# Optimization experiments

Measured on AMD Instinct MI355X. Metric: run time of the kernel, lower is better.

## Reference

```python
import jax, jax.numpy as jnp
import numpy as np

TEMPERATURE = 1.0
N_NODES = 50000
N_EDGES = 1600000
BATCH = 2
C_IN = 64
C_OUT = 64


def setup_inputs() -> dict:
    key = jax.random.key(0)
    k = jax.random.split(key, 8)
    # edge_index with no self-loops: tgt = (src + 1 + off) % N, off in [0, N-2)
    src = jax.random.randint(k[0], (N_EDGES,), 0, N_NODES, dtype=jnp.int64)
    off = jax.random.randint(k[1], (N_EDGES,), 0, N_NODES - 1, dtype=jnp.int64)
    tgt = (src + 1 + off) % N_NODES
    edge_index = jnp.stack([src, tgt])  # (2, E)
    x = jax.random.normal(k[2], (BATCH, N_NODES, C_IN), dtype=jnp.float32)
    f_disc_orig = jax.random.uniform(k[3], (N_EDGES,), dtype=jnp.float32)
    fluxes = jax.random.normal(k[4], (BATCH, N_NODES), dtype=jnp.float32)
    W_conc = jax.random.normal(k[5], (C_OUT, C_IN), dtype=jnp.float32) * (1.0 / np.sqrt(C_IN))
    W_disc = jax.random.normal(k[6], (C_OUT, C_IN), dtype=jnp.float32) * (1.0 / np.sqrt(C_IN))
    bias = jnp.zeros((C_OUT,), dtype=jnp.float32)
    return {"x": x, "edge_index": edge_index, "f_disc_orig": f_disc_orig,
            "fluxes": fluxes, "W_conc": W_conc, "W_disc": W_disc, "bias": bias}


def reference(x, edge_index, f_disc_orig, fluxes, W_conc, W_disc, bias):
    B, N, _ = x.shape
    src0, tgt0 = edge_index[0], edge_index[1]  # original edges (no self-loops)
    loops = jnp.arange(N, dtype=edge_index.dtype)
    src = jnp.concatenate([src0, loops])  # (E+N,)
    tgt = jnp.concatenate([tgt0, loops])
    # GCN symmetric normalization D^{-1/2} A D^{-1/2} (with self-loops)
    deg = jnp.zeros((N,), x.dtype).at[tgt].add(1.0)
    dis = jnp.where(deg > 0, jax.lax.rsqrt(jnp.maximum(deg, 1e-30)), 0.0)
    norm = dis[src] * dis[tgt]  # (E+N,)
    # dynamic discordant strength on original (non-self-loop) edges
    sign_prod = jnp.tanh(fluxes[:, src0] * fluxes[:, tgt0] / TEMPERATURE)  # (B, E)
    keep = (1.0 + sign_prod) * 0.5
    fdo = f_disc_orig[None, :]
    f_disc = keep * fdo + (1.0 - keep) * (1.0 - fdo)  # (B, E)
    # self-loop messages are purely concordant (f_disc = 0)
    f_full = jnp.concatenate([f_disc, jnp.zeros((B, N), x.dtype)], axis=1)  # (B, E+N)
    # transform once per node, then gather per edge
    xc = jnp.einsum('bni,oi->bno', x, W_conc)  # (B, N, O)
    xd = jnp.einsum('bni,oi->bno', x, W_disc)
    msg = norm[None, :, None] * ((1.0 - f_full)[..., None] * xc[:, src] +
                                 f_full[..., None] * xd[:, src])  # (B, E+N, O)
    out = jnp.zeros((B, N, xc.shape[-1]), x.dtype).at[:, tgt].add(msg)
    return out + bias
```

## Files before the change

kernel.cpp:

```cpp
#include <hip/hip_runtime.h>
#include <math.h>


constexpr int C = 64;
constexpr int CNB = 128;
constexpr int CCAP = 5120;

typedef short short8 __attribute__((ext_vector_type(8)));
typedef float f32x4 __attribute__((ext_vector_type(4)));

__device__ __forceinline__ unsigned pack_bf16x2(float a, float b) {
    unsigned ua = __float_as_uint(a);
    ua = (ua + 0x7fffu + ((ua >> 16) & 1u)) >> 16;
    unsigned ub = __float_as_uint(b);
    ub = (ub + 0x7fffu + ((ub >> 16) & 1u)) >> 16;
    return ua | (ub << 16);
}
__device__ __forceinline__ float bflo(unsigned p) { return __uint_as_float(p << 16); }
__device__ __forceinline__ float bfhi(unsigned p) { return __uint_as_float(p & 0xffff0000u); }

__global__ __launch_bounds__(256) void convert_kernel(
    const float* __restrict__ x, unsigned* __restrict__ xb2, int nwords,
    int* __restrict__ coarseCursor, int ncoarse) {
    int i = blockIdx.x * blockDim.x + threadIdx.x;
    if (i < ncoarse) coarseCursor[i] = 0;
    int stride = gridDim.x * blockDim.x;
    const float2* x2 = (const float2*)x;
    for (int w = i; w < nwords; w += stride) {
        float2 xv = x2[w];
        xb2[w] = pack_bf16x2(xv.x, xv.y);
    }
}

__global__ __launch_bounds__(256) void binA1_kernel(
    const int* __restrict__ src, const int* __restrict__ tgt,
    const float* __restrict__ fdo, int* __restrict__ coarseCursor,
    unsigned long long* __restrict__ slab, int E, int ncoarse) {
    __shared__ int hcnt[512];
    __shared__ int hbase[512];
    const int tid = threadIdx.x;
    const int chunk0 = blockIdx.x * 8192;
    for (int c = tid; c < 512; c += 256) hcnt[c] = 0;
    __syncthreads();
#pragma unroll 4
    for (int k = 0; k < 32; ++k) {
        int e = chunk0 + tid + k * 256;
        if (e < E) atomicAdd(&hcnt[tgt[e] >> 7], 1);
    }
    __syncthreads();
    for (int c = tid; c < ncoarse; c += 256) {
        int cc = hcnt[c];
        hbase[c] = cc ? atomicAdd(&coarseCursor[c], cc) : 0;
        hcnt[c] = 0;
    }
    __syncthreads();
#pragma unroll 4
    for (int k = 0; k < 32; ++k) {
        int e = chunk0 + tid + k * 256;
        if (e < E) {
            int t = tgt[e];
            int b = t >> 7;
            int pos = hbase[b] + atomicAdd(&hcnt[b], 1);
            if (pos < CCAP) {
                unsigned q = (unsigned)(fdo[e] * 32767.0f + 0.5f);
                unsigned long long en = (unsigned long long)(unsigned)src[e]
                                      | ((unsigned long long)(unsigned)(t & 127) << 17)
                                      | ((unsigned long long)q << 24);
                slab[(size_t)b * CCAP + pos] = en;
            }
        }
    }
}

__global__ __launch_bounds__(1024) void binA2_kernel(
    const unsigned long long* __restrict__ slab,
    const int* __restrict__ coarseCursor, const float* __restrict__ flux,
    unsigned* __restrict__ epackFine, float4* __restrict__ nodeinfo, int N) {
    const int b = blockIdx.x;
    const int tid = threadIdx.x;
    __shared__ int ncnt[CNB];
    __shared__ int nsc[CNB];
    __shared__ int ncur[CNB];
    int cnt = min(coarseCursor[b], CCAP);
    if (tid < CNB) { ncnt[tid] = 0; ncur[tid] = 0; }
    __syncthreads();
    const unsigned long long* sl = slab + (size_t)b * CCAP;
    for (int i = tid; i < cnt; i += 1024)
        atomicAdd(&ncnt[(int)((sl[i] >> 17) & 127)], 1);
    __syncthreads();
    if (tid < CNB) nsc[tid] = ncnt[tid];
    __syncthreads();
    for (int off = 1; off < CNB; off <<= 1) {
        int v = (tid < CNB && tid >= off) ? nsc[tid - off] : 0;
        __syncthreads();
        if (tid < CNB) nsc[tid] += v;
        __syncthreads();
    }
    for (int i = tid; i < cnt; i += 1024) {
        unsigned long long e = sl[i];
        int s = (int)(e & 0x1FFFFull);
        int tl = (int)((e >> 17) & 127);
        unsigned q = (unsigned)((e >> 24) & 0x7FFF);
        int pos = nsc[tl] - ncnt[tl] + atomicAdd(&ncur[tl], 1);
        epackFine[(size_t)b * CCAP + pos] = (unsigned)s | (q << 17);
    }
    if (tid < CNB) {
        int n = b * CNB + tid;
        if (n < N) {
            int dg = ncnt[tid];
            int rs = b * CCAP + (nsc[tid] - dg);
            float4 ni;
            ni.x = rsqrtf((float)(dg + 1));
            ni.y = flux[n];
            ni.z = flux[N + n];
            ni.w = __int_as_float((dg << 21) | rs);
            nodeinfo[n] = ni;
        }
    }
}

__global__ __launch_bounds__(256) void aggregate_kernel(
    const float4* __restrict__ nodeinfo, const unsigned* __restrict__ epackFine,
    const unsigned* __restrict__ xb2, unsigned* __restrict__ up,
    unsigned* __restrict__ vp, int N) {
    const int lane = threadIdx.x & 63;
    const int wslot = threadIdx.x >> 6;
    const int node = blockIdx.x * 4 + wslot;
    __shared__ float4 s_e[4][2][64];
    if (node >= N) return;
    const int e2 = lane >> 4;
    const int q16 = lane & 15;
    const int g = q16 >> 3;
    const int p = q16 & 7;
    float4 ni = nodeinfo[node];
    const unsigned wbits = (unsigned)__float_as_int(ni.w);
    const int start = (int)(wbits & 0x1FFFFFu);
    const int end = start + (int)(wbits >> 21);
    const float dt = ni.x, f0t = ni.y, f1t = ni.z;
    const char* xbg = (const char*)xb2 + (size_t)g * N * 128 + p * 16;
    float au[8] = {0, 0, 0, 0, 0, 0, 0, 0};
    float av[8] = {0, 0, 0, 0, 0, 0, 0, 0};
    for (int base = start; base < end; base += 64) {
        int cnt = min(64, end - base);
        int cntp = (cnt + 3) & ~3;
        if (lane < cnt) {
            unsigned pe = epackFine[base + lane];
            int s = (int)(pe & 0x1FFFFu);
            float fd = (float)(pe >> 17) * (1.0f / 32767.0f);
            float4 nis = nodeinfo[s];
            float nrm = nis.x * dt;
            float p0 = nis.y * f0t;
            float p1 = nis.z * f1t;
            float k0 = 1.0f / (1.0f + __expf(-2.0f * p0));
            float k1 = 1.0f / (1.0f + __expf(-2.0f * p1));
            float w = 2.0f * fd - 1.0f;
            float f0 = fmaf(k0, w, 1.0f - fd);
            float f1 = fmaf(k1, w, 1.0f - fd);
            float soff = __int_as_float(s << 7);
            s_e[wslot][0][lane] = make_float4(soff, nrm * (1.0f - f0), nrm * f0, 0.f);
            s_e[wslot][1][lane] = make_float4(soff, nrm * (1.0f - f1), nrm * f1, 0.f);
        } else if (lane < cntp) {
            float4 z = make_float4(0.f, 0.f, 0.f, 0.f);
            s_e[wslot][0][lane] = z;
            s_e[wslot][1][lane] = z;
        }
        float4 r0 = s_e[wslot][g][e2];
        uint4 xwN = *(const uint4*)(xbg + __float_as_int(r0.x));
        float ccN = r0.y, cdN = r0.z;
        for (int j = 4; j < cntp; j += 4) {
            uint4 xw = xwN;
            float cc = ccN, cd = cdN;
            float4 r2 = s_e[wslot][g][j + e2];
            xwN = *(const uint4*)(xbg + __float_as_int(r2.x));
            ccN = r2.y; cdN = r2.z;
#pragma unroll
            for (int w = 0; w < 4; ++w) {
                unsigned xp = (&xw.x)[w];
                float lo = bflo(xp), hi = bfhi(xp);
                au[2 * w] = fmaf(cc, lo, au[2 * w]);
                au[2 * w + 1] = fmaf(cc, hi, au[2 * w + 1]);
                av[2 * w] = fmaf(cd, lo, av[2 * w]);
                av[2 * w + 1] = fmaf(cd, hi, av[2 * w + 1]);
            }
        }
#pragma unroll
        for (int w = 0; w < 4; ++w) {
            unsigned xp = (&xwN.x)[w];
            float lo = bflo(xp), hi = bfhi(xp);
            au[2 * w] = fmaf(ccN, lo, au[2 * w]);
            au[2 * w + 1] = fmaf(ccN, hi, au[2 * w + 1]);
            av[2 * w] = fmaf(cdN, lo, av[2 * w]);
            av[2 * w + 1] = fmaf(cdN, hi, av[2 * w + 1]);
        }
    }
#pragma unroll
    for (int k = 0; k < 8; ++k) {
        au[k] += __shfl_xor(au[k], 16, 64);
        au[k] += __shfl_xor(au[k], 32, 64);
        av[k] += __shfl_xor(av[k], 16, 64);
        av[k] += __shfl_xor(av[k], 32, 64);
    }
    if (e2 == 0) {
        uint4 xs = *(const uint4*)(xbg + ((size_t)node << 7));
        float d2 = dt * dt;
#pragma unroll
        for (int w = 0; w < 4; ++w) {
            unsigned xp = (&xs.x)[w];
            au[2 * w] = fmaf(d2, bflo(xp), au[2 * w]);
            au[2 * w + 1] = fmaf(d2, bfhi(xp), au[2 * w + 1]);
        }
        uint4 uo, vo;
        uo.x = pack_bf16x2(au[0], au[1]);
        uo.y = pack_bf16x2(au[2], au[3]);
        uo.z = pack_bf16x2(au[4], au[5]);
        uo.w = pack_bf16x2(au[6], au[7]);
        vo.x = pack_bf16x2(av[0], av[1]);
        vo.y = pack_bf16x2(av[2], av[3]);
        vo.z = pack_bf16x2(av[4], av[5]);
        vo.w = pack_bf16x2(av[6], av[7]);
        size_t wo = ((size_t)(g * N + node)) * 32 + 4 * p;
        *(uint4*)(up + wo) = uo;
        *(uint4*)(vp + wo) = vo;
    }
}

__device__ __forceinline__ short8 make_bfrag(const float* __restrict__ row, int off) {
    const float4* p = (const float4*)(row + off);
    float4 lo = p[0], hi = p[1];
    uint4 w;
    w.x = pack_bf16x2(lo.x, lo.y);
    w.y = pack_bf16x2(lo.z, lo.w);
    w.z = pack_bf16x2(hi.x, hi.y);
    w.w = pack_bf16x2(hi.z, hi.w);
    return __builtin_bit_cast(short8, w);
}

__global__ __launch_bounds__(256) void gemm_mfma_kernel(
    const unsigned* __restrict__ up, const unsigned* __restrict__ vp,
    const float* __restrict__ Wc, const float* __restrict__ Wd,
    const float* __restrict__ bias, float* __restrict__ out, int ntiles) {
    const int lane = threadIdx.x & 63;
    const int nl = lane & 15;
    const int quad = lane >> 4;
    const int wave = blockIdx.x * 4 + (threadIdx.x >> 6);
    const int nwaves = gridDim.x * 4;

    short8 bf[4][4];
    float bt[4];
#pragma unroll
    for (int t = 0; t < 4; ++t) {
        int n = 16 * t + nl;
        const float* wcr = Wc + n * 64;
        const float* wdr = Wd + n * 64;
        bf[0][t] = make_bfrag(wcr, quad * 8);
        bf[1][t] = make_bfrag(wcr, 32 + quad * 8);
        bf[2][t] = make_bfrag(wdr, quad * 8);
        bf[3][t] = make_bfrag(wdr, 32 + quad * 8);
        bt[t] = bias[n];
    }

    for (int tile = wave; tile < ntiles; tile += nwaves) {
        int row = tile * 16 + nl;
        const uint4* ur = (const uint4*)(up + (size_t)row * 32);
        const uint4* vr = (const uint4*)(vp + (size_t)row * 32);
        short8 a0 = __builtin_bit_cast(short8, ur[quad]);
        short8 a1 = __builtin_bit_cast(short8, ur[4 + quad]);
        short8 a2 = __builtin_bit_cast(short8, vr[quad]);
        short8 a3 = __builtin_bit_cast(short8, vr[4 + quad]);
        f32x4 acc[4];
#pragma unroll
        for (int t = 0; t < 4; ++t) {
            f32x4 z = {0.f, 0.f, 0.f, 0.f};
            acc[t] = __builtin_amdgcn_mfma_f32_16x16x32_bf16(a0, bf[0][t], z, 0, 0, 0);
            acc[t] = __builtin_amdgcn_mfma_f32_16x16x32_bf16(a1, bf[1][t], acc[t], 0, 0, 0);
            acc[t] = __builtin_amdgcn_mfma_f32_16x16x32_bf16(a2, bf[2][t], acc[t], 0, 0, 0);
            acc[t] = __builtin_amdgcn_mfma_f32_16x16x32_bf16(a3, bf[3][t], acc[t], 0, 0, 0);
        }
        float* ob = out + ((size_t)(tile * 16 + quad * 4) << 6);
#pragma unroll
        for (int t = 0; t < 4; ++t) {
            int col = 16 * t + nl;
#pragma unroll
            for (int r = 0; r < 4; ++r)
                ob[(r << 6) + col] = acc[t][r] + bt[t];
        }
    }
}

extern "C" void kernel_launch(void* const* d_in, const int* in_sizes, int n_in,
                              void* d_out, int out_size, void* d_ws, size_t ws_size,
                              hipStream_t stream) {
    const float* x = (const float*)d_in[0];
    const int* ei = (const int*)d_in[1];
    const float* fdo = (const float*)d_in[2];
    const float* flux = (const float*)d_in[3];
    const float* Wc = (const float*)d_in[4];
    const float* Wd = (const float*)d_in[5];
    const float* bias = (const float*)d_in[6];
    float* out = (float*)d_out;

    const int E = in_sizes[2];
    const int BN = in_sizes[3];
    const int N = BN / 2;
    const int ncoarse = (N + CNB - 1) / CNB;

    auto align = [](size_t o) { return (o + 255) & ~(size_t)255; };
    char* ws = (char*)d_ws;
    size_t o = 0;
    int* coarseCursor = (int*)(ws + o);            o = align(o + (size_t)ncoarse * 4);
    float4* nodeinfo = (float4*)(ws + o);          o = align(o + (size_t)N * 16);
    unsigned long long* slab = (unsigned long long*)(ws + o);
    unsigned* up = (unsigned*)slab;
    o = align(o + (size_t)ncoarse * CCAP * 8);
    unsigned* epackFine = (unsigned*)(ws + o);     o = align(o + (size_t)ncoarse * CCAP * 4);
    unsigned* xb2 = (unsigned*)(ws + o);           o = align(o + (size_t)BN * 32 * 4);
    unsigned* vp = (unsigned*)(ws + o);            o += (size_t)BN * 32 * 4;

    const int* srcp = ei;
    const int* tgtp = ei + E;

    convert_kernel<<<2048, 256, 0, stream>>>(x, xb2, BN * 32, coarseCursor, ncoarse);
    binA1_kernel<<<(E + 8191) / 8192, 256, 0, stream>>>(srcp, tgtp, fdo,
                                                        coarseCursor, slab, E, ncoarse);
    binA2_kernel<<<ncoarse, 1024, 0, stream>>>(slab, coarseCursor, flux,
                                               epackFine, nodeinfo, N);
    aggregate_kernel<<<(N + 3) / 4, 256, 0, stream>>>(nodeinfo, epackFine, xb2,
                                                      up, vp, N);
    gemm_mfma_kernel<<<512, 256, 0, stream>>>(up, vp, Wc, Wd, bias, out, BN / 16);
}
```

Measured before the change: 220.7 us.

## Interleave batch bf16 rows per node, double gather ILP, shrink blocks

The convert kernel now writes both batch copies of each node contiguously (256 bytes per node), so the two batch gathers in the aggregate kernel hit one contiguous region instead of two distant rows. The aggregate loop processes two edge groups per iteration with two outstanding gather loads, and padding becomes a multiple of 8, to raise memory-level parallelism. Block sizes drop to 128 threads for aggregation and 256 for the fine binning kernel. The convert kernel's reads become strided across batches, and the binning loops run more iterations per thread.

Measured after the change: 225.3 us. 2.1% more time.

```diff
diff --git a/kernel.cpp b/kernel.cpp
--- a/kernel.cpp
+++ b/kernel.cpp
@@ -20,14 +20,18 @@
 __device__ __forceinline__ float bfhi(unsigned p) { return __uint_as_float(p & 0xffff0000u); }
 
 __global__ __launch_bounds__(256) void convert_kernel(
-    const float* __restrict__ x, unsigned* __restrict__ xb2, int nwords,
+    const float* __restrict__ x, unsigned* __restrict__ xb2, int N,
     int* __restrict__ coarseCursor, int ncoarse) {
     int i = blockIdx.x * blockDim.x + threadIdx.x;
     if (i < ncoarse) coarseCursor[i] = 0;
     int stride = gridDim.x * blockDim.x;
     const float2* x2 = (const float2*)x;
+    int nwords = N * 64;
     for (int w = i; w < nwords; w += stride) {
-        float2 xv = x2[w];
+        int node = w >> 6;
+        int g = (w >> 5) & 1;
+        int c = w & 31;
+        float2 xv = x2[((size_t)(g * N + node)) * 32 + c];
         xb2[w] = pack_bf16x2(xv.x, xv.y);
     }
 }
@@ -72,7 +76,7 @@
     }
 }
 
-__global__ __launch_bounds__(1024) void binA2_kernel(
+__global__ __launch_bounds__(256) void binA2_kernel(
     const unsigned long long* __restrict__ slab,
     const int* __restrict__ coarseCursor, const float* __restrict__ flux,
     unsigned* __restrict__ epackFine, float4* __restrict__ nodeinfo, int N) {
@@ -85,7 +89,7 @@
     if (tid < CNB) { ncnt[tid] = 0; ncur[tid] = 0; }
     __syncthreads();
     const unsigned long long* sl = slab + (size_t)b * CCAP;
-    for (int i = tid; i < cnt; i += 1024)
+    for (int i = tid; i < cnt; i += 256)
         atomicAdd(&ncnt[(int)((sl[i] >> 17) & 127)], 1);
     __syncthreads();
     if (tid < CNB) nsc[tid] = ncnt[tid];
@@ -96,7 +100,7 @@
         if (tid < CNB) nsc[tid] += v;
         __syncthreads();
     }
-    for (int i = tid; i < cnt; i += 1024) {
+    for (int i = tid; i < cnt; i += 256) {
         unsigned long long e = sl[i];
         int s = (int)(e & 0x1FFFFull);
         int tl = (int)((e >> 17) & 127);
@@ -119,14 +123,14 @@
     }
 }
 
-__global__ __launch_bounds__(256) void aggregate_kernel(
+__global__ __launch_bounds__(128) void aggregate_kernel(
     const float4* __restrict__ nodeinfo, const unsigned* __restrict__ epackFine,
     const unsigned* __restrict__ xb2, unsigned* __restrict__ up,
     unsigned* __restrict__ vp, int N) {
     const int lane = threadIdx.x & 63;
     const int wslot = threadIdx.x >> 6;
-    const int node = blockIdx.x * 4 + wslot;
-    __shared__ float4 s_e[4][2][64];
+    const int node = blockIdx.x * 2 + wslot;
+    __shared__ float4 s_e[2][2][64];
     if (node >= N) return;
     const int e2 = lane >> 4;
     const int q16 = lane & 15;
@@ -137,12 +141,13 @@
     const int start = (int)(wbits & 0x1FFFFFu);
     const int end = start + (int)(wbits >> 21);
     const float dt = ni.x, f0t = ni.y, f1t = ni.z;
-    const char* xbg = (const char*)xb2 + (size_t)g * N * 128 + p * 16;
+    const char* xbase = (const char*)xb2;
+    const int lane_off = g * 128 + p * 16;
     float au[8] = {0, 0, 0, 0, 0, 0, 0, 0};
     float av[8] = {0, 0, 0, 0, 0, 0, 0, 0};
     for (int base = start; base < end; base += 64) {
         int cnt = min(64, end - base);
-        int cntp = (cnt + 3) & ~3;
+        int cntp = (cnt + 7) & ~7;
         if (lane < cnt) {
             unsigned pe = epackFine[base + lane];
             int s = (int)(pe & 0x1FFFFu);
@@ -156,7 +161,7 @@
             float w = 2.0f * fd - 1.0f;
             float f0 = fmaf(k0, w, 1.0f - fd);
             float f1 = fmaf(k1, w, 1.0f - fd);
-            float soff = __int_as_float(s << 7);
+            float soff = __int_as_float(s << 8);
             s_e[wslot][0][lane] = make_float4(soff, nrm * (1.0f - f0), nrm * f0, 0.f);
             s_e[wslot][1][lane] = make_float4(soff, nrm * (1.0f - f1), nrm * f1, 0.f);
         } else if (lane < cntp) {
@@ -164,33 +169,54 @@
             s_e[wslot][0][lane] = z;
             s_e[wslot][1][lane] = z;
         }
-        float4 r0 = s_e[wslot][g][e2];
-        uint4 xwN = *(const uint4*)(xbg + __float_as_int(r0.x));
-        float ccN = r0.y, cdN = r0.z;
-        for (int j = 4; j < cntp; j += 4) {
-            uint4 xw = xwN;
-            float cc = ccN, cd = cdN;
-            float4 r2 = s_e[wslot][g][j + e2];
-            xwN = *(const uint4*)(xbg + __float_as_int(r2.x));
-            ccN = r2.y; cdN = r2.z;
+        float4 rA = s_e[wslot][g][e2];
+        float4 rB = s_e[wslot][g][4 + e2];
+        uint4 xwA = *(const uint4*)(xbase + (size_t)(unsigned)__float_as_int(rA.x) + lane_off);
+        uint4 xwB = *(const uint4*)(xbase + (size_t)(unsigned)__float_as_int(rB.x) + lane_off);
+        float ccA = rA.y, cdA = rA.z, ccB = rB.y, cdB = rB.z;
+        for (int j = 8; j < cntp; j += 8) {
+            float4 rA2 = s_e[wslot][g][j + e2];
+            float4 rB2 = s_e[wslot][g][j + 4 + e2];
+            uint4 nA = *(const uint4*)(xbase + (size_t)(unsigned)__float_as_int(rA2.x) + lane_off);
+            uint4 nB = *(const uint4*)(xbase + (size_t)(unsigned)__float_as_int(rB2.x) + lane_off);
 #pragma unroll
             for (int w = 0; w < 4; ++w) {
-                unsigned xp = (&xw.x)[w];
+                unsigned xp = (&xwA.x)[w];
                 float lo = bflo(xp), hi = bfhi(xp);
-                au[2 * w] = fmaf(cc, lo, au[2 * w]);
-                au[2 * w + 1] = fmaf(cc, hi, au[2 * w + 1]);
-                av[2 * w] = fmaf(cd, lo, av[2 * w]);
-                av[2 * w + 1] = fmaf(cd, hi, av[2 * w + 1]);
+                au[2 * w] = fmaf(ccA, lo, au[2 * w]);
+                au[2 * w + 1] = fmaf(ccA, hi, au[2 * w + 1]);
+                av[2 * w] = fmaf(cdA, lo, av[2 * w]);
+                av[2 * w + 1] = fmaf(cdA, hi, av[2 * w + 1]);
             }
+#pragma unroll
+            for (int w = 0; w < 4; ++w) {
+                unsigned xp = (&xwB.x)[w];
+                float lo = bflo(xp), hi = bfhi(xp);
+                au[2 * w] = fmaf(ccB, lo, au[2 * w]);
+                au[2 * w + 1] = fmaf(ccB, hi, au[2 * w + 1]);
+                av[2 * w] = fmaf(cdB, lo, av[2 * w]);
+                av[2 * w + 1] = fmaf(cdB, hi, av[2 * w + 1]);
+            }
+            xwA = nA; ccA = rA2.y; cdA = rA2.z;
+            xwB = nB; ccB = rB2.y; cdB = rB2.z;
         }
 #pragma unroll
         for (int w = 0; w < 4; ++w) {
-            unsigned xp = (&xwN.x)[w];
+            unsigned xp = (&xwA.x)[w];
             float lo = bflo(xp), hi = bfhi(xp);
-            au[2 * w] = fmaf(ccN, lo, au[2 * w]);
-            au[2 * w + 1] = fmaf(ccN, hi, au[2 * w + 1]);
-            av[2 * w] = fmaf(cdN, lo, av[2 * w]);
-            av[2 * w + 1] = fmaf(cdN, hi, av[2 * w + 1]);
+            au[2 * w] = fmaf(ccA, lo, au[2 * w]);
+            au[2 * w + 1] = fmaf(ccA, hi, au[2 * w + 1]);
+            av[2 * w] = fmaf(cdA, lo, av[2 * w]);
+            av[2 * w + 1] = fmaf(cdA, hi, av[2 * w + 1]);
+        }
+#pragma unroll
+        for (int w = 0; w < 4; ++w) {
+            unsigned xp = (&xwB.x)[w];
+            float lo = bflo(xp), hi = bfhi(xp);
+            au[2 * w] = fmaf(ccB, lo, au[2 * w]);
+            au[2 * w + 1] = fmaf(ccB, hi, au[2 * w + 1]);
+            av[2 * w] = fmaf(cdB, lo, av[2 * w]);
+            av[2 * w + 1] = fmaf(cdB, hi, av[2 * w + 1]);
         }
     }
 #pragma unroll
@@ -201,7 +227,7 @@
         av[k] += __shfl_xor(av[k], 32, 64);
     }
     if (e2 == 0) {
-        uint4 xs = *(const uint4*)(xbg + ((size_t)node << 7));
+        uint4 xs = *(const uint4*)(xbase + ((size_t)node << 8) + lane_off);
         float d2 = dt * dt;
 #pragma unroll
         for (int w = 0; w < 4; ++w) {
@@ -319,12 +345,12 @@
     const int* srcp = ei;
     const int* tgtp = ei + E;
 
-    convert_kernel<<<2048, 256, 0, stream>>>(x, xb2, BN * 32, coarseCursor, ncoarse);
+    convert_kernel<<<2048, 256, 0, stream>>>(x, xb2, N, coarseCursor, ncoarse);
     binA1_kernel<<<(E + 8191) / 8192, 256, 0, stream>>>(srcp, tgtp, fdo,
                                                         coarseCursor, slab, E, ncoarse);
-    binA2_kernel<<<ncoarse, 1024, 0, stream>>>(slab, coarseCursor, flux,
-                                               epackFine, nodeinfo, N);
-    aggregate_kernel<<<(N + 3) / 4, 256, 0, stream>>>(nodeinfo, epackFine, xb2,
+    binA2_kernel<<<ncoarse, 256, 0, stream>>>(slab, coarseCursor, flux,
+                                              epackFine, nodeinfo, N);
+    aggregate_kernel<<<(N + 1) / 2, 128, 0, stream>>>(nodeinfo, epackFine, xb2,
                                                       up, vp, N);
     gemm_mfma_kernel<<<512, 256, 0, stream>>>(up, vp, Wc, Wd, bias, out, BN / 16);
 }
```

## Fuse fine binning, aggregation and MFMA GEMM into one per-bucket kernel

Applied to the files above, without the earlier changes.

Replaces the separate fine-binning, aggregation and GEMM kernels with one mega kernel per 64-node bucket. It sorts edges in LDS, aggregates into LDS-resident bf16 u/v rows, and runs the MFMA projection directly from shared memory. Degrees now come from a global atomic pass fused with the bf16 conversion, whose layout interleaves both batches per node so one gather serves both. Edge coefficients are packed to bf16 in staging. This removes the epackFine and u/v global round trips and two launches, but adds global atomics for degree, a memset, and a large-LDS kernel that may limit occupancy.

Result: slower. 326.0 us (+47.7%).

```diff
diff --git a/kernel.cpp b/kernel.cpp
--- a/kernel.cpp
+++ b/kernel.cpp
@@ -2,9 +2,8 @@
 #include <math.h>
 
 
-constexpr int C = 64;
-constexpr int CNB = 128;
-constexpr int CCAP = 5120;
+constexpr int SNB = 64;
+constexpr int SCAP = 2560;
 
 typedef short short8 __attribute__((ext_vector_type(8)));
 typedef float f32x4 __attribute__((ext_vector_type(4)));
@@ -19,33 +18,51 @@
 __device__ __forceinline__ float bflo(unsigned p) { return __uint_as_float(p << 16); }
 __device__ __forceinline__ float bfhi(unsigned p) { return __uint_as_float(p & 0xffff0000u); }
 
-__global__ __launch_bounds__(256) void convert_kernel(
-    const float* __restrict__ x, unsigned* __restrict__ xb2, int nwords,
-    int* __restrict__ coarseCursor, int ncoarse) {
-    int i = blockIdx.x * blockDim.x + threadIdx.x;
-    if (i < ncoarse) coarseCursor[i] = 0;
-    int stride = gridDim.x * blockDim.x;
+__global__ __launch_bounds__(256) void conv_deg_kernel(
+    const float* __restrict__ x, unsigned* __restrict__ xb2, int N,
+    const int* __restrict__ tgt, int E, int* __restrict__ deg) {
+    int i = blockIdx.x * 256 + threadIdx.x;
+    int stride = gridDim.x * 256;
+    for (int e = i; e < E; e += stride) atomicAdd(&deg[tgt[e]], 1);
     const float2* x2 = (const float2*)x;
+    int nwords = N * 64;
     for (int w = i; w < nwords; w += stride) {
-        float2 xv = x2[w];
+        int node = w >> 6, g = (w >> 5) & 1, c = w & 31;
+        float2 xv = x2[((size_t)(g * N + node)) * 32 + c];
         xb2[w] = pack_bf16x2(xv.x, xv.y);
     }
 }
 
-__global__ __launch_bounds__(256) void binA1_kernel(
+__global__ __launch_bounds__(256) void binA1_ni_kernel(
     const int* __restrict__ src, const int* __restrict__ tgt,
     const float* __restrict__ fdo, int* __restrict__ coarseCursor,
-    unsigned long long* __restrict__ slab, int E, int ncoarse) {
-    __shared__ int hcnt[512];
-    __shared__ int hbase[512];
+    unsigned long long* __restrict__ slab, int E, int ncoarse, int nb1,
+    const int* __restrict__ deg, const float* __restrict__ flux,
+    float4* __restrict__ nodeinfo, int N) {
+    if ((int)blockIdx.x >= nb1) {
+        int i = ((int)blockIdx.x - nb1) * 256 + threadIdx.x;
+        int stride = (gridDim.x - nb1) * 256;
+        for (int n = i; n < N; n += stride) {
+            float dis = rsqrtf((float)(deg[n] + 1));
+            float4 ni;
+            ni.x = dis;
+            ni.y = flux[n];
+            ni.z = flux[N + n];
+            ni.w = dis * dis;
+            nodeinfo[n] = ni;
+        }
+        return;
+    }
+    __shared__ int hcnt[1024];
+    __shared__ int hbase[1024];
     const int tid = threadIdx.x;
     const int chunk0 = blockIdx.x * 8192;
-    for (int c = tid; c < 512; c += 256) hcnt[c] = 0;
+    for (int c = tid; c < 1024; c += 256) hcnt[c] = 0;
     __syncthreads();
 #pragma unroll 4
     for (int k = 0; k < 32; ++k) {
         int e = chunk0 + tid + k * 256;
-        if (e < E) atomicAdd(&hcnt[tgt[e] >> 7], 1);
+        if (e < E) atomicAdd(&hcnt[tgt[e] >> 6], 1);
     }
     __syncthreads();
     for (int c = tid; c < ncoarse; c += 256) {
@@ -59,230 +76,227 @@
         int e = chunk0 + tid + k * 256;
         if (e < E) {
             int t = tgt[e];
-            int b = t >> 7;
+            int b = t >> 6;
             int pos = hbase[b] + atomicAdd(&hcnt[b], 1);
-            if (pos < CCAP) {
+            if (pos < SCAP) {
                 unsigned q = (unsigned)(fdo[e] * 32767.0f + 0.5f);
                 unsigned long long en = (unsigned long long)(unsigned)src[e]
-                                      | ((unsigned long long)(unsigned)(t & 127) << 17)
-                                      | ((unsigned long long)q << 24);
-                slab[(size_t)b * CCAP + pos] = en;
-            }
-        }
-    }
-}
-
-__global__ __launch_bounds__(1024) void binA2_kernel(
+                                      | ((unsigned long long)(unsigned)(t & 63) << 17)
+                                      | ((unsigned long long)q << 23);
+                slab[(size_t)b * SCAP + pos] = en;
+            }
+        }
+    }
+}
+
+__global__ __launch_bounds__(512, 4) void mega_kernel(
     const unsigned long long* __restrict__ slab,
-    const int* __restrict__ coarseCursor, const float* __restrict__ flux,
-    unsigned* __restrict__ epackFine, float4* __restrict__ nodeinfo, int N) {
+    const int* __restrict__ coarseCursor, const float4* __restrict__ nodeinfo,
+    const unsigned* __restrict__ xb2, const float* __restrict__ Wc,
+    const float* __restrict__ Wd, const float* __restrict__ bias,
+    float* __restrict__ out, int N) {
     const int b = blockIdx.x;
     const int tid = threadIdx.x;
-    __shared__ int ncnt[CNB];
-    __shared__ int nsc[CNB];
-    __shared__ int ncur[CNB];
-    int cnt = min(coarseCursor[b], CCAP);
-    if (tid < CNB) { ncnt[tid] = 0; ncur[tid] = 0; }
-    __syncthreads();
-    const unsigned long long* sl = slab + (size_t)b * CCAP;
-    for (int i = tid; i < cnt; i += 1024)
-        atomicAdd(&ncnt[(int)((sl[i] >> 17) & 127)], 1);
-    __syncthreads();
-    if (tid < CNB) nsc[tid] = ncnt[tid];
-    __syncthreads();
-    for (int off = 1; off < CNB; off <<= 1) {
-        int v = (tid < CNB && tid >= off) ? nsc[tid - off] : 0;
+    const int lane = tid & 63;
+    const int w = tid >> 6;
+    __shared__ int fcnt[SNB], fstart[SNB], fcur[SNB], ftmp[SNB];
+    __shared__ unsigned fine[SCAP];
+    __shared__ uint2 stag[8][2][64];
+    __shared__ unsigned short uv[2 * SNB][136];
+
+    int cnt = min(coarseCursor[b], SCAP);
+    if (tid < SNB) { fcnt[tid] = 0; fcur[tid] = 0; }
+    __syncthreads();
+    const unsigned long long* sl = slab + (size_t)b * SCAP;
+    unsigned long long ent[5];
+    int ne = 0;
+    for (int i = tid; i < cnt; i += 512) {
+        ent[ne] = sl[i];
+        atomicAdd(&fcnt[(int)((ent[ne] >> 17) & 63)], 1);
+        ++ne;
+    }
+    __syncthreads();
+    if (tid < SNB) ftmp[tid] = fcnt[tid];
+    __syncthreads();
+    for (int off = 1; off < SNB; off <<= 1) {
+        int v = (tid < SNB && tid >= off) ? ftmp[tid - off] : 0;
         __syncthreads();
-        if (tid < CNB) nsc[tid] += v;
+        if (tid < SNB) ftmp[tid] += v;
         __syncthreads();
     }
-    for (int i = tid; i < cnt; i += 1024) {
-        unsigned long long e = sl[i];
-        int s = (int)(e & 0x1FFFFull);
-        int tl = (int)((e >> 17) & 127);
-        unsigned q = (unsigned)((e >> 24) & 0x7FFF);
-        int pos = nsc[tl] - ncnt[tl] + atomicAdd(&ncur[tl], 1);
-        epackFine[(size_t)b * CCAP + pos] = (unsigned)s | (q << 17);
-    }
-    if (tid < CNB) {
-        int n = b * CNB + tid;
-        if (n < N) {
-            int dg = ncnt[tid];
-            int rs = b * CCAP + (nsc[tid] - dg);
-            float4 ni;
-            ni.x = rsqrtf((float)(dg + 1));
-            ni.y = flux[n];
-            ni.z = flux[N + n];
-            ni.w = __int_as_float((dg << 21) | rs);
-            nodeinfo[n] = ni;
-        }
-    }
-}
-
-__global__ __launch_bounds__(256) void aggregate_kernel(
-    const float4* __restrict__ nodeinfo, const unsigned* __restrict__ epackFine,
-    const unsigned* __restrict__ xb2, unsigned* __restrict__ up,
-    unsigned* __restrict__ vp, int N) {
-    const int lane = threadIdx.x & 63;
-    const int wslot = threadIdx.x >> 6;
-    const int node = blockIdx.x * 4 + wslot;
-    __shared__ float4 s_e[4][2][64];
-    if (node >= N) return;
+    if (tid < SNB) fstart[tid] = ftmp[tid] - fcnt[tid];
+    __syncthreads();
+    for (int k = 0; k < ne; ++k) {
+        unsigned long long e = ent[k];
+        int tl = (int)((e >> 17) & 63);
+        int pos = fstart[tl] + atomicAdd(&fcur[tl], 1);
+        fine[pos] = (unsigned)(e & 0x1FFFFull) | ((unsigned)((e >> 23) & 0x7FFF) << 17);
+    }
+    __syncthreads();
+
     const int e2 = lane >> 4;
     const int q16 = lane & 15;
     const int g = q16 >> 3;
     const int p = q16 & 7;
-    float4 ni = nodeinfo[node];
-    const unsigned wbits = (unsigned)__float_as_int(ni.w);
-    const int start = (int)(wbits & 0x1FFFFFu);
-    const int end = start + (int)(wbits >> 21);
-    const float dt = ni.x, f0t = ni.y, f1t = ni.z;
-    const char* xbg = (const char*)xb2 + (size_t)g * N * 128 + p * 16;
-    float au[8] = {0, 0, 0, 0, 0, 0, 0, 0};
-    float av[8] = {0, 0, 0, 0, 0, 0, 0, 0};
-    for (int base = start; base < end; base += 64) {
-        int cnt = min(64, end - base);
-        int cntp = (cnt + 3) & ~3;
-        if (lane < cnt) {
-            unsigned pe = epackFine[base + lane];
-            int s = (int)(pe & 0x1FFFFu);
-            float fd = (float)(pe >> 17) * (1.0f / 32767.0f);
-            float4 nis = nodeinfo[s];
-            float nrm = nis.x * dt;
-            float p0 = nis.y * f0t;
-            float p1 = nis.z * f1t;
-            float k0 = 1.0f / (1.0f + __expf(-2.0f * p0));
-            float k1 = 1.0f / (1.0f + __expf(-2.0f * p1));
-            float w = 2.0f * fd - 1.0f;
-            float f0 = fmaf(k0, w, 1.0f - fd);
-            float f1 = fmaf(k1, w, 1.0f - fd);
-            float soff = __int_as_float(s << 7);
-            s_e[wslot][0][lane] = make_float4(soff, nrm * (1.0f - f0), nrm * f0, 0.f);
-            s_e[wslot][1][lane] = make_float4(soff, nrm * (1.0f - f1), nrm * f1, 0.f);
-        } else if (lane < cntp) {
-            float4 z = make_float4(0.f, 0.f, 0.f, 0.f);
-            s_e[wslot][0][lane] = z;
-            s_e[wslot][1][lane] = z;
-        }
-        float4 r0 = s_e[wslot][g][e2];
-        uint4 xwN = *(const uint4*)(xbg + __float_as_int(r0.x));
-        float ccN = r0.y, cdN = r0.z;
-        for (int j = 4; j < cntp; j += 4) {
-            uint4 xw = xwN;
-            float cc = ccN, cd = cdN;
-            float4 r2 = s_e[wslot][g][j + e2];
-            xwN = *(const uint4*)(xbg + __float_as_int(r2.x));
-            ccN = r2.y; cdN = r2.z;
-#pragma unroll
-            for (int w = 0; w < 4; ++w) {
-                unsigned xp = (&xw.x)[w];
+    const char* xbase = (const char*)xb2;
+    const int lane_off = g * 128 + p * 16;
+    for (int k8 = 0; k8 < 8; ++k8) {
+        const int nl_ = w + 8 * k8;
+        const int node = b * SNB + nl_;
+        float4 ni = (node < N) ? nodeinfo[node] : make_float4(0.f, 0.f, 0.f, 0.f);
+        const float dt = ni.x, f0t = ni.y, f1t = ni.z;
+        const int start = fstart[nl_];
+        const int end = start + fcnt[nl_];
+        float au[8] = {0, 0, 0, 0, 0, 0, 0, 0};
+        float av[8] = {0, 0, 0, 0, 0, 0, 0, 0};
+        for (int base = start; base < end; base += 64) {
+            int c64 = min(64, end - base);
+            int cp = (c64 + 3) & ~3;
+            if (lane < c64) {
+                unsigned fe = fine[base + lane];
+                int s = (int)(fe & 0x1FFFFu);
+                float fd = (float)(fe >> 17) * (1.0f / 32767.0f);
+                float4 nis = nodeinfo[s];
+                float nrm = nis.x * dt;
+                float p0 = nis.y * f0t;
+                float p1 = nis.z * f1t;
+                float k0 = 1.0f / (1.0f + __expf(-2.0f * p0));
+                float k1 = 1.0f / (1.0f + __expf(-2.0f * p1));
+                float ww = 2.0f * fd - 1.0f;
+                float f0 = fmaf(k0, ww, 1.0f - fd);
+                float f1 = fmaf(k1, ww, 1.0f - fd);
+                stag[w][0][lane] = make_uint2((unsigned)(s << 8),
+                                              pack_bf16x2(nrm * (1.0f - f0), nrm * f0));
+                stag[w][1][lane] = make_uint2((unsigned)(s << 8),
+                                              pack_bf16x2(nrm * (1.0f - f1), nrm * f1));
+            } else if (lane < cp) {
+                stag[w][0][lane] = make_uint2(0u, 0u);
+                stag[w][1][lane] = make_uint2(0u, 0u);
+            }
+            uint2 r0 = stag[w][g][e2];
+            uint4 xw = *(const uint4*)(xbase + r0.x + lane_off);
+            float cc = bflo(r0.y), cd = bfhi(r0.y);
+            for (int j = 4; j < cp; j += 4) {
+                uint2 r2 = stag[w][g][j + e2];
+                uint4 nx = *(const uint4*)(xbase + r2.x + lane_off);
+#pragma unroll
+                for (int q = 0; q < 4; ++q) {
+                    unsigned xp = (&xw.x)[q];
+                    float lo = bflo(xp), hi = bfhi(xp);
+                    au[2 * q] = fmaf(cc, lo, au[2 * q]);
+                    au[2 * q + 1] = fmaf(cc, hi, au[2 * q + 1]);
+                    av[2 * q] = fmaf(cd, lo, av[2 * q]);
+                    av[2 * q + 1] = fmaf(cd, hi, av[2 * q + 1]);
+                }
+                xw = nx;
+                cc = bflo(r2.y);
+                cd = bfhi(r2.y);
+            }
+#pragma unroll
+            for (int q = 0; q < 4; ++q) {
+                unsigned xp = (&xw.x)[q];
                 float lo = bflo(xp), hi = bfhi(xp);
-                au[2 * w] = fmaf(cc, lo, au[2 * w]);
-                au[2 * w + 1] = fmaf(cc, hi, au[2 * w + 1]);
-                av[2 * w] = fmaf(cd, lo, av[2 * w]);
-                av[2 * w + 1] = fmaf(cd, hi, av[2 * w + 1]);
-            }
-        }
-#pragma unroll
-        for (int w = 0; w < 4; ++w) {
-            unsigned xp = (&xwN.x)[w];
-            float lo = bflo(xp), hi = bfhi(xp);
-            au[2 * w] = fmaf(ccN, lo, au[2 * w]);
-            au[2 * w + 1] = fmaf(ccN, hi, au[2 * w + 1]);
-            av[2 * w] = fmaf(cdN, lo, av[2 * w]);
-            av[2 * w + 1] = fmaf(cdN, hi, av[2 * w + 1]);
-        }
-    }
-#pragma unroll
-    for (int k = 0; k < 8; ++k) {
-        au[k] += __shfl_xor(au[k], 16, 64);
-        au[k] += __shfl_xor(au[k], 32, 64);
-        av[k] += __shfl_xor(av[k], 16, 64);
-        av[k] += __shfl_xor(av[k], 32, 64);
-    }
-    if (e2 == 0) {
-        uint4 xs = *(const uint4*)(xbg + ((size_t)node << 7));
-        float d2 = dt * dt;
-#pragma unroll
-        for (int w = 0; w < 4; ++w) {
-            unsigned xp = (&xs.x)[w];
-            au[2 * w] = fmaf(d2, bflo(xp), au[2 * w]);
-            au[2 * w + 1] = fmaf(d2, bfhi(xp), au[2 * w + 1]);
-        }
-        uint4 uo, vo;
-        uo.x = pack_bf16x2(au[0], au[1]);
-        uo.y = pack_bf16x2(au[2], au[3]);
-        uo.z = pack_bf16x2(au[4], au[5]);
-        uo.w = pack_bf16x2(au[6], au[7]);
-        vo.x = pack_bf16x2(av[0], av[1]);
-        vo.y = pack_bf16x2(av[2], av[3]);
-        vo.z = pack_bf16x2(av[4], av[5]);
-        vo.w = pack_bf16x2(av[6], av[7]);
-        size_t wo = ((size_t)(g * N + node)) * 32 + 4 * p;
-        *(uint4*)(up + wo) = uo;
-        *(uint4*)(vp + wo) = vo;
-    }
-}
-
-__device__ __forceinline__ short8 make_bfrag(const float* __restrict__ row, int off) {
-    const float4* p = (const float4*)(row + off);
-    float4 lo = p[0], hi = p[1];
-    uint4 w;
-    w.x = pack_bf16x2(lo.x, lo.y);
-    w.y = pack_bf16x2(lo.z, lo.w);
-    w.z = pack_bf16x2(hi.x, hi.y);
-    w.w = pack_bf16x2(hi.z, hi.w);
-    return __builtin_bit_cast(short8, w);
-}
-
-__global__ __launch_bounds__(256) void gemm_mfma_kernel(
-    const unsigned* __restrict__ up, const unsigned* __restrict__ vp,
-    const float* __restrict__ Wc, const float* __restrict__ Wd,
-    const float* __restrict__ bias, float* __restrict__ out, int ntiles) {
-    const int lane = threadIdx.x & 63;
-    const int nl = lane & 15;
-    const int quad = lane >> 4;
-    const int wave = blockIdx.x * 4 + (threadIdx.x >> 6);
-    const int nwaves = gridDim.x * 4;
-
+                au[2 * q] = fmaf(cc, lo, au[2 * q]);
+                au[2 * q + 1] = fmaf(cc, hi, au[2 * q + 1]);
+                av[2 * q] = fmaf(cd, lo, av[2 * q]);
+                av[2 * q + 1] = fmaf(cd, hi, av[2 * q + 1]);
+            }
+        }
+#pragma unroll
+        for (int k = 0; k < 8; ++k) {
+            au[k] += __shfl_xor(au[k], 16, 64);
+            au[k] += __shfl_xor(au[k], 32, 64);
+            av[k] += __shfl_xor(av[k], 16, 64);
+            av[k] += __shfl_xor(av[k], 32, 64);
+        }
+        if (e2 == 0) {
+            if (node < N) {
+                uint4 xs = *(const uint4*)(xbase + ((size_t)node << 8) + lane_off);
+                float d2 = ni.w;
+#pragma unroll
+                for (int q = 0; q < 4; ++q) {
+                    unsigned xp = (&xs.x)[q];
+                    au[2 * q] = fmaf(d2, bflo(xp), au[2 * q]);
+                    au[2 * q + 1] = fmaf(d2, bfhi(xp), au[2 * q + 1]);
+                }
+            }
+            uint4 uo, vo;
+            uo.x = pack_bf16x2(au[0], au[1]);
+            uo.y = pack_bf16x2(au[2], au[3]);
+            uo.z = pack_bf16x2(au[4], au[5]);
+            uo.w = pack_bf16x2(au[6], au[7]);
+            vo.x = pack_bf16x2(av[0], av[1]);
+            vo.y = pack_bf16x2(av[2], av[3]);
+            vo.z = pack_bf16x2(av[4], av[5]);
+            vo.w = pack_bf16x2(av[6], av[7]);
+            int r = g * SNB + nl_;
+            *(uint4*)&uv[r][p * 8] = uo;
+            *(uint4*)&uv[r][64 + p * 8] = vo;
+        }
+    }
+    __syncthreads();
+
+    const int nl = lane & 15, quad = lane >> 4;
     short8 bf[4][4];
     float bt[4];
 #pragma unroll
-    for (int t = 0; t < 4; ++t) {
-        int n = 16 * t + nl;
+    for (int tt = 0; tt < 4; ++tt) {
+        int n = 16 * tt + nl;
         const float* wcr = Wc + n * 64;
         const float* wdr = Wd + n * 64;
-        bf[0][t] = make_bfrag(wcr, quad * 8);
-        bf[1][t] = make_bfrag(wcr, 32 + quad * 8);
-        bf[2][t] = make_bfrag(wdr, quad * 8);
-        bf[3][t] = make_bfrag(wdr, 32 + quad * 8);
-        bt[t] = bias[n];
-    }
-
-    for (int tile = wave; tile < ntiles; tile += nwaves) {
-        int row = tile * 16 + nl;
-        const uint4* ur = (const uint4*)(up + (size_t)row * 32);
-        const uint4* vr = (const uint4*)(vp + (size_t)row * 32);
-        short8 a0 = __builtin_bit_cast(short8, ur[quad]);
-        short8 a1 = __builtin_bit_cast(short8, ur[4 + quad]);
-        short8 a2 = __builtin_bit_cast(short8, vr[quad]);
-        short8 a3 = __builtin_bit_cast(short8, vr[4 + quad]);
-        f32x4 acc[4];
-#pragma unroll
-        for (int t = 0; t < 4; ++t) {
-            f32x4 z = {0.f, 0.f, 0.f, 0.f};
-            acc[t] = __builtin_amdgcn_mfma_f32_16x16x32_bf16(a0, bf[0][t], z, 0, 0, 0);
-            acc[t] = __builtin_amdgcn_mfma_f32_16x16x32_bf16(a1, bf[1][t], acc[t], 0, 0, 0);
-            acc[t] = __builtin_amdgcn_mfma_f32_16x16x32_bf16(a2, bf[2][t], acc[t], 0, 0, 0);
-            acc[t] = __builtin_amdgcn_mfma_f32_16x16x32_bf16(a3, bf[3][t], acc[t], 0, 0, 0);
-        }
-        float* ob = out + ((size_t)(tile * 16 + quad * 4) << 6);
-#pragma unroll
-        for (int t = 0; t < 4; ++t) {
-            int col = 16 * t + nl;
-#pragma unroll
-            for (int r = 0; r < 4; ++r)
-                ob[(r << 6) + col] = acc[t][r] + bt[t];
+        const float4* pc0 = (const float4*)(wcr + quad * 8);
+        const float4* pc1 = (const float4*)(wcr + 32 + quad * 8);
+        const float4* pd0 = (const float4*)(wdr + quad * 8);
+        const float4* pd1 = (const float4*)(wdr + 32 + quad * 8);
+        float4 a, bb;
+        uint4 wv;
+        a = pc0[0]; bb = pc0[1];
+        wv.x = pack_bf16x2(a.x, a.y); wv.y = pack_bf16x2(a.z, a.w);
+        wv.z = pack_bf16x2(bb.x, bb.y); wv.w = pack_bf16x2(bb.z, bb.w);
+        bf[0][tt] = __builtin_bit_cast(short8, wv);
+        a = pc1[0]; bb = pc1[1];
+        wv.x = pack_bf16x2(a.x, a.y); wv.y = pack_bf16x2(a.z, a.w);
+        wv.z = pack_bf16x2(bb.x, bb.y); wv.w = pack_bf16x2(bb.z, bb.w);
+        bf[1][tt] = __builtin_bit_cast(short8, wv);
+        a = pd0[0]; bb = pd0[1];
+        wv.x = pack_bf16x2(a.x, a.y); wv.y = pack_bf16x2(a.z, a.w);
+        wv.z = pack_bf16x2(bb.x, bb.y); wv.w = pack_bf16x2(bb.z, bb.w);
+        bf[2][tt] = __builtin_bit_cast(short8, wv);
+        a = pd1[0]; bb = pd1[1];
+        wv.x = pack_bf16x2(a.x, a.y); wv.y = pack_bf16x2(a.z, a.w);
+        wv.z = pack_bf16x2(bb.x, bb.y); wv.w = pack_bf16x2(bb.z, bb.w);
+        bf[3][tt] = __builtin_bit_cast(short8, wv);
+        bt[tt] = bias[n];
+    }
+    const int t = w;
+    const int r = 16 * t + nl;
+    uint4 afr[4];
+#pragma unroll
+    for (int kk = 0; kk < 4; ++kk)
+        afr[kk] = *(const uint4*)&uv[r][kk * 32 + quad * 8];
+    f32x4 acc[4];
+#pragma unroll
+    for (int tt = 0; tt < 4; ++tt) {
+        f32x4 z = {0.f, 0.f, 0.f, 0.f};
+        acc[tt] = __builtin_amdgcn_mfma_f32_16x16x32_bf16(
+            __builtin_bit_cast(short8, afr[0]), bf[0][tt], z, 0, 0, 0);
+        acc[tt] = __builtin_amdgcn_mfma_f32_16x16x32_bf16(
+            __builtin_bit_cast(short8, afr[1]), bf[1][tt], acc[tt], 0, 0, 0);
+        acc[tt] = __builtin_amdgcn_mfma_f32_16x16x32_bf16(
+            __builtin_bit_cast(short8, afr[2]), bf[2][tt], acc[tt], 0, 0, 0);
+        acc[tt] = __builtin_amdgcn_mfma_f32_16x16x32_bf16(
+            __builtin_bit_cast(short8, afr[3]), bf[3][tt], acc[tt], 0, 0, 0);
+    }
+    const int gg = t >> 2;
+    const int nlb = (t & 3) * 16 + quad * 4;
+#pragma unroll
+    for (int tt = 0; tt < 4; ++tt) {
+        int col = 16 * tt + nl;
+#pragma unroll
+        for (int rr = 0; rr < 4; ++rr) {
+            int node = b * SNB + nlb + rr;
+            if (node < N)
+                out[(((size_t)(gg * N + node)) << 6) + col] = acc[tt][rr] + bt[tt];
         }
     }
 }
@@ -302,29 +316,28 @@
     const int E = in_sizes[2];
     const int BN = in_sizes[3];
     const int N = BN / 2;
-    const int ncoarse = (N + CNB - 1) / CNB;
+    const int ncoarse = (N + SNB - 1) / SNB;
 
     auto align = [](size_t o) { return (o + 255) & ~(size_t)255; };
     char* ws = (char*)d_ws;
     size_t o = 0;
-    int* coarseCursor = (int*)(ws + o);            o = align(o + (size_t)ncoarse * 4);
-    float4* nodeinfo = (float4*)(ws + o);          o = align(o + (size_t)N * 16);
+    int* deg = (int*)(ws + o);            o += (size_t)N * 4;
+    int* coarseCursor = (int*)(ws + o);   o = align(o + (size_t)ncoarse * 4);
+    size_t zero_end = o;
+    float4* nodeinfo = (float4*)(ws + o); o = align(o + (size_t)N * 16);
     unsigned long long* slab = (unsigned long long*)(ws + o);
-    unsigned* up = (unsigned*)slab;
-    o = align(o + (size_t)ncoarse * CCAP * 8);
-    unsigned* epackFine = (unsigned*)(ws + o);     o = align(o + (size_t)ncoarse * CCAP * 4);
-    unsigned* xb2 = (unsigned*)(ws + o);           o = align(o + (size_t)BN * 32 * 4);
-    unsigned* vp = (unsigned*)(ws + o);            o += (size_t)BN * 32 * 4;
+    o = align(o + (size_t)ncoarse * SCAP * 8);
+    unsigned* xb2 = (unsigned*)(ws + o);  o = align(o + (size_t)BN * 32 * 4);
 
     const int* srcp = ei;
     const int* tgtp = ei + E;
 
-    convert_kernel<<<2048, 256, 0, stream>>>(x, xb2, BN * 32, coarseCursor, ncoarse);
-    binA1_kernel<<<(E + 8191) / 8192, 256, 0, stream>>>(srcp, tgtp, fdo,
-                                                        coarseCursor, slab, E, ncoarse);
-    binA2_kernel<<<ncoarse, 1024, 0, stream>>>(slab, coarseCursor, flux,
-                                               epackFine, nodeinfo, N);
-    aggregate_kernel<<<(N + 3) / 4, 256, 0, stream>>>(nodeinfo, epackFine, xb2,
-                                                      up, vp, N);
-    gemm_mfma_kernel<<<512, 256, 0, stream>>>(up, vp, Wc, Wd, bias, out, BN / 16);
-}
+    hipMemsetAsync(ws, 0, zero_end, stream);
+    conv_deg_kernel<<<2048, 256, 0, stream>>>(x, xb2, N, tgtp, E, deg);
+    int nb1 = (E + 8191) / 8192;
+    binA1_ni_kernel<<<nb1 + 64, 256, 0, stream>>>(srcp, tgtp, fdo, coarseCursor,
+                                                  slab, E, ncoarse, nb1, deg,
+                                                  flux, nodeinfo, N);
+    mega_kernel<<<ncoarse, 512, 0, stream>>>(slab, coarseCursor, nodeinfo, xb2,
+                                             Wc, Wd, bias, out, N);
+}
```
